# Performance work log

Measured on AMD Instinct MI355X. Metric: run time of the kernel, lower is better.

The kernel has to match this reference:

```python
import jax, jax.numpy as jnp
import numpy as np

N_NODES = 50000
N_EDGES = 300000
INPUT_DIM = 128
HIDDEN_DIM = 256
NUM_HEADS = 8
HEAD_DIM = HIDDEN_DIM // NUM_HEADS  # 32
NUM_EDGE_TYPES = 3


def setup_inputs() -> dict:
    key = jax.random.key(0)
    ks = jax.random.split(key, 12)
    s_in = 1.0 / np.sqrt(INPUT_DIM)
    s_hid = 1.0 / np.sqrt(HIDDEN_DIM)
    return {
        "node_features": jax.random.normal(ks[0], (N_NODES, INPUT_DIM), jnp.float32),
        "edges": jax.random.randint(ks[1], (N_EDGES, 2), 0, N_NODES),
        "edge_types": jax.random.randint(ks[2], (N_EDGES,), 0, NUM_EDGE_TYPES),
        # torch.nn.Linear convention: y = x @ W.T + b, W: [out, in]
        "Wq": jax.random.normal(ks[3], (HIDDEN_DIM, INPUT_DIM), jnp.float32) * s_in,
        "bq": jax.random.normal(ks[4], (HIDDEN_DIM,), jnp.float32) * s_in,
        "Wk": jax.random.normal(ks[5], (HIDDEN_DIM, INPUT_DIM), jnp.float32) * s_in,
        "bk": jax.random.normal(ks[6], (HIDDEN_DIM,), jnp.float32) * s_in,
        "Wv": jax.random.normal(ks[7], (HIDDEN_DIM, INPUT_DIM), jnp.float32) * s_in,
        "bv": jax.random.normal(ks[8], (HIDDEN_DIM,), jnp.float32) * s_in,
        "edge_emb": jax.random.normal(ks[9], (NUM_EDGE_TYPES, HIDDEN_DIM), jnp.float32),
        "Wo": jax.random.normal(ks[10], (INPUT_DIM, HIDDEN_DIM), jnp.float32) * s_hid,
        "bo": jax.random.normal(ks[11], (INPUT_DIM,), jnp.float32) * s_hid,
    }


def reference(node_features, edges, edge_types, Wq, bq, Wk, bk, Wv, bv, edge_emb, Wo, bo):
    # Project all nodes once, split heads: [N, H, D]
    Q = (node_features @ Wq.T + bq).reshape(-1, NUM_HEADS, HEAD_DIM)
    K = (node_features @ Wk.T + bk).reshape(-1, NUM_HEADS, HEAD_DIM)
    V = (node_features @ Wv.T + bv).reshape(-1, NUM_HEADS, HEAD_DIM)

    src = edges[:, 0]
    tgt = edges[:, 1]

    # Per-edge small attention: Q[src] [E,H,D] x K[tgt]^T -> [E,H,H]
    # (identical math to the original per-edge-type loop, since only the
    #  edge embedding depends on edge_type and it is gathered per edge)
    scale = 1.0 / jnp.sqrt(jnp.float32(HEAD_DIM))
    scores = jnp.einsum("ehd,egd->ehg", Q[src], K[tgt]) * scale
    attn = jax.nn.softmax(scores, axis=-1)
    msg = jnp.einsum("ehg,egd->ehd", attn, V[tgt]).reshape(-1, HIDDEN_DIM)  # [E, HID]

    msg = msg + edge_emb[edge_types]          # per-edge-type embedding add
    out_e = msg @ Wo.T + bo                   # output projection per edge [E, IN]

    # Scatter-add over source nodes (original Python loop over edges)
    messages = jax.ops.segment_sum(out_e, src, num_segments=N_NODES)
    return messages
```

## Files before the change

### kernel.cpp

```cpp
#include <hip/hip_runtime.h>
#include <hip/hip_bf16.h>

#define N_NODES 50000
#define N_EDGES 300000
#define M_PAD 50048
#define M_PAD2 50176
#define NBLK 196
#define SC 0.17677669529663687f

#define MB_CONV 6250
#define MB_HIST 1172
#define MB_PREP 513

#define QKV_BLOCKS 2346
#define SCAT_BLOCKS 586

typedef __attribute__((ext_vector_type(8))) short bf16x8;
typedef __attribute__((ext_vector_type(4))) short bf16x4;
typedef __attribute__((ext_vector_type(4))) float f32x4;

typedef __attribute__((address_space(3))) unsigned int lds_uint;
typedef const __attribute__((address_space(1))) unsigned int glb_uint;
__device__ __forceinline__ void gld16(const void* g, void* l) {
    __builtin_amdgcn_global_load_lds((glb_uint*)g, (lds_uint*)l, 16, 0, 0);
}

__device__ __forceinline__ unsigned short f2bf(float x) {
    unsigned int u = __float_as_uint(x);
    unsigned int r = (u + 0x7FFFu + ((u >> 16) & 1u)) >> 16;
    return (unsigned short)r;
}
__device__ __forceinline__ short bfs(float x) {
    __hip_bfloat16 h = __float2bfloat16(x);
    return *reinterpret_cast<short*>(&h);
}

__global__ __launch_bounds__(512)
void qkv_gemm(const unsigned short* __restrict__ A2, const unsigned short* __restrict__ B2,
              const float* __restrict__ biasCat,
              unsigned short* __restrict__ Qb, unsigned short* __restrict__ Kb,
              unsigned short* __restrict__ Vb,
              const int* __restrict__ edges, int* __restrict__ cursor,
              int* __restrict__ packed)
{
    __shared__ unsigned short SMEM[128 * 128];
    const int bid = blockIdx.x;
    const int t   = threadIdx.x;

    if (bid >= QKV_BLOCKS) {
        const int e = (bid - QKV_BLOCKS) * 512 + t;
        if (e < N_EDGES) {
            const int pos = atomicAdd(&cursor[edges[2 * e]], 1);
            packed[pos] = edges[2 * e + 1];
        }
        return;
    }

    const int w    = t >> 6;
    const int lane = t & 63;
    const int l15  = lane & 15;
    const int lg   = lane >> 4;
    const int mt   = bid % 6;
    const int mat  = mt % 3;
    const int nh   = mt / 3;
    const int m0   = (bid / 6) * 128;
    const int wm   = (w >> 2) * 64;
    const int wn   = (w & 3) * 32;
    const float mulc = (mat == 0) ? SC : 1.0f;

    {
        const char* srcbase = (const char*)A2 + (size_t)m0 * 256;
        #pragma unroll
        for (int i = 0; i < 4; ++i) {
            const int cb = (i * 8 + w) * 1024;
            gld16(srcbase + cb + lane * 16, (char*)SMEM + cb);
        }
    }

    f32x4 acc[4][2] = {};
    const unsigned short* Bbase =
        B2 + (size_t)(mat * 256 + nh * 128 + wn + l15) * 128 + lg * 8;

    __syncthreads();

    #pragma unroll
    for (int ks = 0; ks < 4; ++ks) {
        bf16x8 af[4], bfv[2];
        #pragma unroll
        for (int ni = 0; ni < 2; ++ni)
            bfv[ni] = *(const bf16x8*)(Bbase + (size_t)ni * 16 * 128 + ks * 32);
        #pragma unroll
        for (int mi = 0; mi < 4; ++mi) {
            const int r    = wm + mi * 16 + l15;
            const int slot = (ks * 4 + lg) ^ ((r & 7) << 1);
            af[mi] = *(const bf16x8*)((const char*)SMEM + r * 256 + slot * 16);
        }
        #pragma unroll
        for (int mi = 0; mi < 4; ++mi)
            #pragma unroll
            for (int ni = 0; ni < 2; ++ni)
                acc[mi][ni] = __builtin_amdgcn_mfma_f32_16x16x32_bf16(
                    af[mi], bfv[ni], acc[mi][ni], 0, 0, 0);
    }

    __syncthreads();

    unsigned short* Cs = SMEM;
    float bvn[2];
    #pragma unroll
    for (int ni = 0; ni < 2; ++ni)
        bvn[ni] = biasCat[mat * 256 + nh * 128 + wn + ni * 16 + l15];

    #pragma unroll
    for (int mi = 0; mi < 4; ++mi)
        #pragma unroll
        for (int j = 0; j < 4; ++j) {
            const int row = wm + mi * 16 + lg * 4 + j;
            const int xr  = (row & 7) << 3;
            #pragma unroll
            for (int ni = 0; ni < 2; ++ni) {
                const int col = wn + ni * 16 + l15;
                Cs[row * 128 + (col ^ xr)] = f2bf(fmaf(acc[mi][ni][j], mulc, bvn[ni]));
            }
        }
    __syncthreads();

    if (mat < 2) {
        unsigned short* dst = mat ? Kb : Qb;
        #pragma unroll
        for (int c8 = 0; c8 < 4; ++c8) {
            const int chunk = c8 * 512 + t;
            const int row = chunk >> 4;
            const int ec  = (chunk & 15) * 8;
            const bf16x8 v = *(const bf16x8*)&Cs[row * 128 + (ec ^ ((row & 7) << 3))];
            *(bf16x8*)&dst[(size_t)(m0 + row) * 256 + nh * 128 + ec] = v;
        }
    } else {
        #pragma unroll
        for (int i8 = 0; i8 < 8; ++i8) {
            const int item = i8 * 512 + t;
            const int row  = item >> 5;
            const int d    = item & 31;
            const int xr   = (row & 7) << 3;
            bf16x4 v;
            #pragma unroll
            for (int g = 0; g < 4; ++g)
                v[g] = (short)Cs[row * 128 + ((g * 32 + d) ^ xr)];
            *(bf16x4*)&Vb[(size_t)(m0 + row) * 256 + d * 8 + nh * 4] = v;
        }
    }
}

__global__ __launch_bounds__(128)
void out_gemm(const unsigned short* __restrict__ accQ, const unsigned short* __restrict__ B2o,
              const float* __restrict__ eew, const float* __restrict__ bo,
              const float4* __restrict__ cnt4, float* __restrict__ Cout)
{
    const int t    = threadIdx.x;
    const int w    = t >> 6;
    const int lane = t & 63;
    const int l15  = lane & 15;
    const int lg   = lane >> 4;
    const int m0   = blockIdx.y * 32;
    const int wn   = w * 64;

    f32x4 acc[2][4] = {};

    const unsigned short* Abase = accQ + (size_t)(m0 + l15) * 256 + lg * 8;
    const unsigned short* Bbase = B2o + (size_t)(wn + l15) * 256 + lg * 8;

    #pragma unroll 2
    for (int ks = 0; ks < 8; ++ks) {
        bf16x8 af[2], bfv[4];
        #pragma unroll
        for (int mi = 0; mi < 2; ++mi)
            af[mi] = *(const bf16x8*)(Abase + (size_t)mi * 16 * 256 + ks * 32);
        #pragma unroll
        for (int ni = 0; ni < 4; ++ni)
            bfv[ni] = *(const bf16x8*)(Bbase + (size_t)ni * 16 * 256 + ks * 32);
        #pragma unroll
        for (int mi = 0; mi < 2; ++mi)
            #pragma unroll
            for (int ni = 0; ni < 4; ++ni)
                acc[mi][ni] = __builtin_amdgcn_mfma_f32_16x16x32_bf16(
                    af[mi], bfv[ni], acc[mi][ni], 0, 0, 0);
    }

    #pragma unroll
    for (int mi = 0; mi < 2; ++mi)
        #pragma unroll
        for (int j = 0; j < 4; ++j) {
            const int row = m0 + mi * 16 + lg * 4 + j;
            if (row < N_NODES) {
                const float4 cv = cnt4[row];
                #pragma unroll
                for (int ni = 0; ni < 4; ++ni) {
                    const int col = wn + ni * 16 + l15;
                    Cout[(size_t)row * 128 + col] = acc[mi][ni][j]
                        + cv.x * eew[col] + cv.y * eew[128 + col]
                        + cv.z * eew[256 + col] + cv.w * bo[col];
                }
            }
        }
}

__global__ __launch_bounds__(256)
void mega_prep(const float4* __restrict__ nf4,
               const int* __restrict__ edges, const int* __restrict__ etypes,
               const float* __restrict__ Wq, const float* __restrict__ Wk,
               const float* __restrict__ Wv, const float* __restrict__ bq,
               const float* __restrict__ bk, const float* __restrict__ bv,
               const float* __restrict__ Wo, const float* __restrict__ ee,
               unsigned short* __restrict__ A2, unsigned short* __restrict__ B2qkv,
               unsigned short* __restrict__ B2o,
               float* __restrict__ biasCat, float* __restrict__ eew,
               int* __restrict__ degType)
{
    const int bid = blockIdx.x, t = threadIdx.x;
    if (bid < MB_CONV) {
        const int tid = bid * 256 + t;
        const int m = tid >> 5, k4 = (tid & 31) * 4;
        const float4 v = nf4[tid];
        ushort4 hi;
        hi.x = f2bf(v.x); hi.y = f2bf(v.y); hi.z = f2bf(v.z); hi.w = f2bf(v.w);
        const int chunk = k4 >> 3;
        const int sub   = k4 & 7;
        const int scol  = ((chunk ^ ((m & 7) << 1)) << 3) + sub;
        *reinterpret_cast<ushort4*>(&A2[(size_t)m * 128 + scol]) = hi;
    } else if (bid < MB_CONV + MB_HIST) {
        const int e = (bid - MB_CONV) * 256 + t;
        if (e < N_EDGES) atomicAdd(&degType[edges[2 * e] * 4 + etypes[e]], 1);
    } else {
        const int pbid = bid - MB_CONV - MB_HIST;
        if (pbid < 384) {
            const int tid = pbid * 256 + t;
            const int r = tid >> 7, k = tid & 127;
            const float* W = (r < 256) ? Wq : (r < 512) ? Wk : Wv;
            B2qkv[(size_t)r * 128 + k] = f2bf(W[(size_t)(r & 255) * 128 + k]);
            if (k == 0) {
                const float* b = (r < 256) ? bq : (r < 512) ? bk : bv;
                biasCat[r] = b[r & 255] * ((r < 256) ? SC : 1.0f);
            }
        } else if (pbid < 512) {
            const int tid = (pbid - 384) * 256 + t;
            const int r = tid >> 8, k = tid & 255;
            B2o[(size_t)r * 256 + k] = f2bf(Wo[(size_t)r * 256 + k]);
        } else if (t < 128) {
            float a0 = 0.f, a1 = 0.f, a2 = 0.f;
            for (int k = 0; k < 256; ++k) {
                const float w = Wo[(size_t)t * 256 + k];
                a0 += ee[k] * w; a1 += ee[256 + k] * w; a2 += ee[512 + k] * w;
            }
            eew[t] = a0; eew[128 + t] = a1; eew[256 + t] = a2;
        }
    }
}

__global__ __launch_bounds__(256)
void scan_part1(const int4* __restrict__ degType4, int* __restrict__ blockSum)
{
    const int t = threadIdx.x;
    const int i = blockIdx.x * 256 + t;
    int v = 0;
    if (i < N_NODES) {
        const int4 dt = degType4[i];
        v = dt.x + dt.y + dt.z;
    }
    #pragma unroll
    for (int o = 1; o < 64; o <<= 1) v += __shfl_xor(v, o);
    __shared__ int ws[4];
    if ((t & 63) == 0) ws[t >> 6] = v;
    __syncthreads();
    if (t == 0) blockSum[blockIdx.x] = ws[0] + ws[1] + ws[2] + ws[3];
}

__global__ __launch_bounds__(256)
void scan_part2(const int* __restrict__ blockSum, int* __restrict__ blockBase,
                int* __restrict__ rowStart)
{
    __shared__ int lds[256];
    const int t = threadIdx.x;
    lds[t] = (t < NBLK) ? blockSum[t] : 0;
    __syncthreads();
    #pragma unroll
    for (int o = 1; o < 256; o <<= 1) {
        const int u = (t >= o) ? lds[t - o] : 0;
        __syncthreads();
        lds[t] += u;
        __syncthreads();
    }
    if (t < NBLK) blockBase[t] = (t == 0) ? 0 : lds[t - 1];
    if (t == 0) rowStart[N_NODES] = N_EDGES;
}

__global__ __launch_bounds__(256)
void scan_part3(const int4* __restrict__ degType4, const int* __restrict__ blockBase,
                int* __restrict__ rowStart, int* __restrict__ cursor,
                float4* __restrict__ cnt4)
{
    const int t = threadIdx.x;
    const int lane = t & 63, wid = t >> 6;
    const int i = blockIdx.x * 256 + t;
    int4 dt = make_int4(0, 0, 0, 0);
    if (i < N_NODES) dt = degType4[i];
    const int d = dt.x + dt.y + dt.z;
    int x = d;
    #pragma unroll
    for (int o = 1; o < 64; o <<= 1) {
        const int u = __shfl_up(x, o);
        if (lane >= o) x += u;
    }
    __shared__ int wtot[4];
    if (lane == 63) wtot[wid] = x;
    __syncthreads();
    int wo = 0;
    #pragma unroll
    for (int wi = 0; wi < 3; ++wi) wo += (wi < wid) ? wtot[wi] : 0;
    const int excl = blockBase[blockIdx.x] + wo + x - d;
    if (i < N_NODES) {
        rowStart[i] = excl;
        cursor[i]   = excl;
        cnt4[i]     = make_float4((float)dt.x, (float)dt.y, (float)dt.z, (float)d);
    }
}

__device__ __forceinline__ bf16x4 softmax_pa(f32x4 s, bool valid)
{
    const float e0 = __expf(s[0]), e1 = __expf(s[1]);
    const float e2 = __expf(s[2]), e3 = __expf(s[3]);
    float sum = e0 + e1 + e2 + e3;
    sum += __shfl_xor(sum, 16);
    const float inv = valid ? __builtin_amdgcn_rcpf(sum) : 0.0f;
    bf16x4 pa;
    pa[0] = bfs(e0 * inv);
    pa[1] = bfs(e1 * inv);
    pa[2] = bfs(e2 * inv);
    pa[3] = bfs(e3 * inv);
    return pa;
}

__global__ __launch_bounds__(256)
void node_gather_kernel(const int* __restrict__ packed, const int* __restrict__ rowStart,
                        const unsigned short* __restrict__ Qb,
                        const unsigned short* __restrict__ Kb,
                        const unsigned short* __restrict__ Vb,
                        unsigned short* __restrict__ accQ)
{
    const int lane = threadIdx.x & 63;
    const int n = blockIdx.x * 4 + (threadIdx.x >> 6);
    if (n >= N_NODES) return;
    const int l15 = lane & 15;
    const int lg  = lane >> 4;

    const bf16x8 qf = *(const bf16x8*)&Qb[(size_t)n * 256 + (l15 & 7) * 32 + lg * 8];

    f32x4 cpvA0 = {0.f,0.f,0.f,0.f}, cpvA1 = {0.f,0.f,0.f,0.f};
    f32x4 cpvB0 = {0.f,0.f,0.f,0.f}, cpvB1 = {0.f,0.f,0.f,0.f};

    const int lo = rowStart[n], hi = rowStart[n + 1];
    const bool validBase = ((l15 < 8) == (lg < 2));
    const f32x4 z4 = {0.f, 0.f, 0.f, 0.f};
    int idx = lo;

    for (; idx + 4 <= hi; idx += 4) {
        const int t0 = packed[idx],     t1 = packed[idx + 1];
        const int t2 = packed[idx + 2], t3 = packed[idx + 3];

        const int tkA = (l15 < 8) ? t0 : t1;
        const int tkB = (l15 < 8) ? t2 : t3;
        const bf16x8 kfA = *(const bf16x8*)&Kb[(size_t)tkA * 256 + (l15 & 7) * 32 + lg * 8];
        const bf16x8 kfB = *(const bf16x8*)&Kb[(size_t)tkB * 256 + (l15 & 7) * 32 + lg * 8];

        const int tvA = (lg < 2) ? t0 : t1;
        const int tvB = (lg < 2) ? t2 : t3;
        const unsigned short* vrA = &Vb[(size_t)tvA * 256 + (lg & 1) * 4];
        const unsigned short* vrB = &Vb[(size_t)tvB * 256 + (lg & 1) * 4];
        const bf16x4 vfA0 = *(const bf16x4*)&vrA[l15 * 8];
        const bf16x4 vfA1 = *(const bf16x4*)&vrA[(l15 + 16) * 8];
        const bf16x4 vfB0 = *(const bf16x4*)&vrB[l15 * 8];
        const bf16x4 vfB1 = *(const bf16x4*)&vrB[(l15 + 16) * 8];

        const f32x4 sA = __builtin_amdgcn_mfma_f32_16x16x32_bf16(kfA, qf, z4, 0, 0, 0);
        const f32x4 sB = __builtin_amdgcn_mfma_f32_16x16x32_bf16(kfB, qf, z4, 0, 0, 0);

        const bf16x4 paA = softmax_pa(sA, validBase);
        const bf16x4 paB = softmax_pa(sB, validBase);

        cpvA0 = __builtin_amdgcn_mfma_f32_16x16x16bf16_1k(paA, vfA0, cpvA0, 0, 0, 0);
        cpvA1 = __builtin_amdgcn_mfma_f32_16x16x16bf16_1k(paA, vfA1, cpvA1, 0, 0, 0);
        cpvB0 = __builtin_amdgcn_mfma_f32_16x16x16bf16_1k(paB, vfB0, cpvB0, 0, 0, 0);
        cpvB1 = __builtin_amdgcn_mfma_f32_16x16x16bf16_1k(paB, vfB1, cpvB1, 0, 0, 0);
    }

    for (; idx < hi; idx += 2) {
        const int  t0  = packed[idx];
        const bool dup = (idx + 1 >= hi);
        const int  t1  = dup ? t0 : packed[idx + 1];

        const int tk = (l15 < 8) ? t0 : t1;
        const bf16x8 kf = *(const bf16x8*)&Kb[(size_t)tk * 256 + (l15 & 7) * 32 + lg * 8];

        const int tv = (lg < 2) ? t0 : t1;
        const unsigned short* vrow = &Vb[(size_t)tv * 256 + (lg & 1) * 4];
        const bf16x4 vf0 = *(const bf16x4*)&vrow[l15 * 8];
        const bf16x4 vf1 = *(const bf16x4*)&vrow[(l15 + 16) * 8];

        const f32x4 s = __builtin_amdgcn_mfma_f32_16x16x32_bf16(kf, qf, z4, 0, 0, 0);
        const bool valid = validBase && !(dup && (l15 >= 8));
        const bf16x4 pa = softmax_pa(s, valid);

        cpvA0 = __builtin_amdgcn_mfma_f32_16x16x16bf16_1k(pa, vf0, cpvA0, 0, 0, 0);
        cpvA1 = __builtin_amdgcn_mfma_f32_16x16x16bf16_1k(pa, vf1, cpvA1, 0, 0, 0);
    }

    f32x4 cpv0 = cpvA0 + cpvB0;
    f32x4 cpv1 = cpvA1 + cpvB1;

    #pragma unroll
    for (int j = 0; j < 4; ++j) {
        cpv0[j] += __shfl_xor(cpv0[j], 32);
        cpv1[j] += __shfl_xor(cpv1[j], 32);
    }

    if (lane < 32) {
        unsigned short* row = &accQ[(size_t)n * 256];
        #pragma unroll
        for (int j = 0; j < 4; ++j) {
            const int h = lg * 4 + j;
            row[h * 32 + l15]      = (unsigned short)bfs(cpv0[j]);
            row[h * 32 + 16 + l15] = (unsigned short)bfs(cpv1[j]);
        }
    }
}

extern "C" void kernel_launch(void* const* d_in, const int* in_sizes, int n_in,
                              void* d_out, int out_size, void* d_ws, size_t ws_size,
                              hipStream_t stream)
{
    const float* nf      = (const float*)d_in[0];
    const int*   edges   = (const int*)d_in[1];
    const int*   etypes  = (const int*)d_in[2];
    const float* Wq      = (const float*)d_in[3];
    const float* bq      = (const float*)d_in[4];
    const float* Wk      = (const float*)d_in[5];
    const float* bk      = (const float*)d_in[6];
    const float* Wv      = (const float*)d_in[7];
    const float* bv      = (const float*)d_in[8];
    const float* ee      = (const float*)d_in[9];
    const float* Wo      = (const float*)d_in[10];
    const float* bo      = (const float*)d_in[11];
    float* out = (float*)d_out;

    char* ws = (char*)d_ws;
    size_t off = 0;
    auto alloc = [&](size_t bytes) -> void* {
        void* p = ws + off;
        off = (off + bytes + 255) & ~(size_t)255;
        return p;
    };
    unsigned short* A2     = (unsigned short*)alloc((size_t)M_PAD * 128 * 2);
    unsigned short* B2qkv  = (unsigned short*)alloc((size_t)768 * 128 * 2);
    unsigned short* B2o    = (unsigned short*)alloc((size_t)128 * 256 * 2);
    float*          biasC  = (float*)alloc(768 * sizeof(float));
    float*          eew    = (float*)alloc(384 * sizeof(float));
    unsigned short* Qb     = (unsigned short*)alloc((size_t)M_PAD * 256 * 2);
    unsigned short* Kb     = (unsigned short*)alloc((size_t)M_PAD * 256 * 2);
    unsigned short* Vb     = (unsigned short*)alloc((size_t)M_PAD * 256 * 2);
    unsigned short* accQ   = (unsigned short*)alloc((size_t)M_PAD2 * 256 * 2);
    float4* cnt4    = (float4*)alloc((size_t)N_NODES * sizeof(float4));
    int*    degType = (int*)alloc((size_t)N_NODES * 4 * sizeof(int));
    int*    rowS    = (int*)alloc((size_t)(N_NODES + 1) * sizeof(int));
    int*    curs    = (int*)alloc((size_t)N_NODES * sizeof(int));
    int*    pck     = (int*)alloc((size_t)N_EDGES * sizeof(int));
    int*    bSum    = (int*)alloc((size_t)NBLK * sizeof(int));
    int*    bBase   = (int*)alloc((size_t)NBLK * sizeof(int));

    const dim3 blk(256);

    hipMemsetAsync(degType, 0, (size_t)N_NODES * 4 * sizeof(int), stream);
    mega_prep<<<dim3(MB_CONV + MB_HIST + MB_PREP), blk, 0, stream>>>(
        (const float4*)nf, edges, etypes, Wq, Wk, Wv, bq, bk, bv, Wo, ee,
        A2, B2qkv, B2o, biasC, eew, degType);

    scan_part1<<<dim3(NBLK), blk, 0, stream>>>((const int4*)degType, bSum);
    scan_part2<<<dim3(1), blk, 0, stream>>>(bSum, bBase, rowS);
    scan_part3<<<dim3(NBLK), blk, 0, stream>>>((const int4*)degType, bBase, rowS, curs, cnt4);

    qkv_gemm<<<dim3(QKV_BLOCKS + SCAT_BLOCKS), dim3(512), 0, stream>>>(
        A2, B2qkv, biasC, Qb, Kb, Vb, edges, curs, pck);

    node_gather_kernel<<<dim3((N_NODES + 3) / 4), blk, 0, stream>>>(
        pck, rowS, Qb, Kb, Vb, accQ);

    out_gemm<<<dim3(1, M_PAD2 / 32), dim3(128), 0, stream>>>(
        accQ, B2o, eew, bo, cnt4, out);
}
```

Measured before the change: 161.5 us.

## Loop all six QKV tiles per 64-row block and repack V for 16-byte gathers

New measurement: 162.7 us. Within noise of the previous version (+0.7%).

```diff
diff --git a/kernel.cpp b/kernel.cpp
--- a/kernel.cpp
+++ b/kernel.cpp
@@ -12,7 +12,7 @@
 #define MB_HIST 1172
 #define MB_PREP 513
 
-#define QKV_BLOCKS 2346
+#define QKV_BLOCKS 782
 #define SCAT_BLOCKS 586
 
 typedef __attribute__((ext_vector_type(8))) short bf16x8;
@@ -43,7 +43,8 @@
               const int* __restrict__ edges, int* __restrict__ cursor,
               int* __restrict__ packed)
 {
-    __shared__ unsigned short SMEM[128 * 128];
+    __shared__ unsigned short A_s[64 * 128];
+    __shared__ unsigned short C_s[64 * 128];
     const int bid = blockIdx.x;
     const int t   = threadIdx.x;
 
@@ -60,93 +61,77 @@
     const int lane = t & 63;
     const int l15  = lane & 15;
     const int lg   = lane >> 4;
-    const int mt   = bid % 6;
-    const int mat  = mt % 3;
-    const int nh   = mt / 3;
-    const int m0   = (bid / 6) * 128;
-    const int wm   = (w >> 2) * 64;
-    const int wn   = (w & 3) * 32;
-    const float mulc = (mat == 0) ? SC : 1.0f;
+    const int m0   = bid * 64;
+    const int wn   = w * 16;
 
     {
         const char* srcbase = (const char*)A2 + (size_t)m0 * 256;
-        #pragma unroll
-        for (int i = 0; i < 4; ++i) {
-            const int cb = (i * 8 + w) * 1024;
-            gld16(srcbase + cb + lane * 16, (char*)SMEM + cb);
-        }
-    }
-
-    f32x4 acc[4][2] = {};
-    const unsigned short* Bbase =
-        B2 + (size_t)(mat * 256 + nh * 128 + wn + l15) * 128 + lg * 8;
-
+        gld16(srcbase + t * 16,              (char*)A_s + t * 16);
+        gld16(srcbase + (512 + t) * 16,      (char*)A_s + (512 + t) * 16);
+    }
     __syncthreads();
 
     #pragma unroll
-    for (int ks = 0; ks < 4; ++ks) {
-        bf16x8 af[4], bfv[2];
-        #pragma unroll
-        for (int ni = 0; ni < 2; ++ni)
-            bfv[ni] = *(const bf16x8*)(Bbase + (size_t)ni * 16 * 128 + ks * 32);
-        #pragma unroll
-        for (int mi = 0; mi < 4; ++mi) {
-            const int r    = wm + mi * 16 + l15;
-            const int slot = (ks * 4 + lg) ^ ((r & 7) << 1);
-            af[mi] = *(const bf16x8*)((const char*)SMEM + r * 256 + slot * 16);
-        }
+    for (int mt = 0; mt < 6; ++mt) {
+        const int mat = mt >> 1;
+        const int nh  = mt & 1;
+        const float mulc = (mat == 0) ? SC : 1.0f;
+        const float bvn  = biasCat[mat * 256 + nh * 128 + wn + l15];
+        const unsigned short* Bbase =
+            B2 + (size_t)(mat * 256 + nh * 128 + wn + l15) * 128 + lg * 8;
+
+        f32x4 acc[4] = {};
+        #pragma unroll
+        for (int ks = 0; ks < 4; ++ks) {
+            const bf16x8 bfv = *(const bf16x8*)(Bbase + ks * 32);
+            #pragma unroll
+            for (int mi = 0; mi < 4; ++mi) {
+                const int r    = mi * 16 + l15;
+                const int slot = (ks * 4 + lg) ^ ((r & 7) << 1);
+                const bf16x8 af = *(const bf16x8*)((const char*)A_s + r * 256 + slot * 16);
+                acc[mi] = __builtin_amdgcn_mfma_f32_16x16x32_bf16(af, bfv, acc[mi], 0, 0, 0);
+            }
+        }
+
+        __syncthreads();
+
         #pragma unroll
         for (int mi = 0; mi < 4; ++mi)
             #pragma unroll
-            for (int ni = 0; ni < 2; ++ni)
-                acc[mi][ni] = __builtin_amdgcn_mfma_f32_16x16x32_bf16(
-                    af[mi], bfv[ni], acc[mi][ni], 0, 0, 0);
-    }
-
-    __syncthreads();
-
-    unsigned short* Cs = SMEM;
-    float bvn[2];
-    #pragma unroll
-    for (int ni = 0; ni < 2; ++ni)
-        bvn[ni] = biasCat[mat * 256 + nh * 128 + wn + ni * 16 + l15];
-
-    #pragma unroll
-    for (int mi = 0; mi < 4; ++mi)
-        #pragma unroll
-        for (int j = 0; j < 4; ++j) {
-            const int row = wm + mi * 16 + lg * 4 + j;
-            const int xr  = (row & 7) << 3;
+            for (int j = 0; j < 4; ++j) {
+                const int row = mi * 16 + lg * 4 + j;
+                const int xr  = (row & 7) << 3;
+                const int col = wn + l15;
+                C_s[row * 128 + (col ^ xr)] = f2bf(fmaf(acc[mi][j], mulc, bvn));
+            }
+        __syncthreads();
+
+        if (mat < 2) {
+            unsigned short* dst = mat ? Kb : Qb;
             #pragma unroll
-            for (int ni = 0; ni < 2; ++ni) {
-                const int col = wn + ni * 16 + l15;
-                Cs[row * 128 + (col ^ xr)] = f2bf(fmaf(acc[mi][ni][j], mulc, bvn[ni]));
-            }
-        }
-    __syncthreads();
-
-    if (mat < 2) {
-        unsigned short* dst = mat ? Kb : Qb;
-        #pragma unroll
-        for (int c8 = 0; c8 < 4; ++c8) {
-            const int chunk = c8 * 512 + t;
-            const int row = chunk >> 4;
-            const int ec  = (chunk & 15) * 8;
-            const bf16x8 v = *(const bf16x8*)&Cs[row * 128 + (ec ^ ((row & 7) << 3))];
-            *(bf16x8*)&dst[(size_t)(m0 + row) * 256 + nh * 128 + ec] = v;
-        }
-    } else {
-        #pragma unroll
-        for (int i8 = 0; i8 < 8; ++i8) {
-            const int item = i8 * 512 + t;
-            const int row  = item >> 5;
-            const int d    = item & 31;
-            const int xr   = (row & 7) << 3;
-            bf16x4 v;
+            for (int c8 = 0; c8 < 2; ++c8) {
+                const int chunk = c8 * 512 + t;
+                const int row = chunk >> 4;
+                const int ec  = (chunk & 15) * 8;
+                const bf16x8 v = *(const bf16x8*)&C_s[row * 128 + (ec ^ ((row & 7) << 3))];
+                *(bf16x8*)&dst[(size_t)(m0 + row) * 256 + nh * 128 + ec] = v;
+            }
+        } else {
             #pragma unroll
-            for (int g = 0; g < 4; ++g)
-                v[g] = (short)Cs[row * 128 + ((g * 32 + d) ^ xr)];
-            *(bf16x4*)&Vb[(size_t)(m0 + row) * 256 + d * 8 + nh * 4] = v;
+            for (int c8 = 0; c8 < 2; ++c8) {
+                const int item = c8 * 512 + t;
+                const int row  = item >> 4;
+                const int dlow = item & 15;
+                const int xr   = (row & 7) << 3;
+                bf16x8 v;
+                #pragma unroll
+                for (int jp = 0; jp < 8; ++jp) {
+                    const int dhi = jp >> 2, gp = jp & 3;
+                    const int cp  = gp * 32 + dlow + 16 * dhi;
+                    v[jp] = (short)C_s[row * 128 + (cp ^ xr)];
+                }
+                *(bf16x8*)&Vb[(size_t)(m0 + row) * 256 + nh * 128 + dlow * 8] = v;
+            }
         }
     }
 }
@@ -339,6 +324,8 @@
     return pa;
 }
 
+union v8split { bf16x8 v8; bf16x4 h[2]; };
+
 __global__ __launch_bounds__(256)
 void node_gather_kernel(const int* __restrict__ packed, const int* __restrict__ rowStart,
                         const unsigned short* __restrict__ Qb,
@@ -360,6 +347,7 @@
     const int lo = rowStart[n], hi = rowStart[n + 1];
     const bool validBase = ((l15 < 8) == (lg < 2));
     const f32x4 z4 = {0.f, 0.f, 0.f, 0.f};
+    const int voff = (lg & 1) * 128 + l15 * 8;
     int idx = lo;
 
     for (; idx + 4 <= hi; idx += 4) {
@@ -373,12 +361,9 @@
 
         const int tvA = (lg < 2) ? t0 : t1;
         const int tvB = (lg < 2) ? t2 : t3;
-        const unsigned short* vrA = &Vb[(size_t)tvA * 256 + (lg & 1) * 4];
-        const unsigned short* vrB = &Vb[(size_t)tvB * 256 + (lg & 1) * 4];
-        const bf16x4 vfA0 = *(const bf16x4*)&vrA[l15 * 8];
-        const bf16x4 vfA1 = *(const bf16x4*)&vrA[(l15 + 16) * 8];
-        const bf16x4 vfB0 = *(const bf16x4*)&vrB[l15 * 8];
-        const bf16x4 vfB1 = *(const bf16x4*)&vrB[(l15 + 16) * 8];
+        v8split vA, vB;
+        vA.v8 = *(const bf16x8*)&Vb[(size_t)tvA * 256 + voff];
+        vB.v8 = *(const bf16x8*)&Vb[(size_t)tvB * 256 + voff];
 
         const f32x4 sA = __builtin_amdgcn_mfma_f32_16x16x32_bf16(kfA, qf, z4, 0, 0, 0);
         const f32x4 sB = __builtin_amdgcn_mfma_f32_16x16x32_bf16(kfB, qf, z4, 0, 0, 0);
@@ -386,10 +371,10 @@
         const bf16x4 paA = softmax_pa(sA, validBase);
         const bf16x4 paB = softmax_pa(sB, validBase);
 
-        cpvA0 = __builtin_amdgcn_mfma_f32_16x16x16bf16_1k(paA, vfA0, cpvA0, 0, 0, 0);
-        cpvA1 = __builtin_amdgcn_mfma_f32_16x16x16bf16_1k(paA, vfA1, cpvA1, 0, 0, 0);
-        cpvB0 = __builtin_amdgcn_mfma_f32_16x16x16bf16_1k(paB, vfB0, cpvB0, 0, 0, 0);
-        cpvB1 = __builtin_amdgcn_mfma_f32_16x16x16bf16_1k(paB, vfB1, cpvB1, 0, 0, 0);
+        cpvA0 = __builtin_amdgcn_mfma_f32_16x16x16bf16_1k(paA, vA.h[0], cpvA0, 0, 0, 0);
+        cpvA1 = __builtin_amdgcn_mfma_f32_16x16x16bf16_1k(paA, vA.h[1], cpvA1, 0, 0, 0);
+        cpvB0 = __builtin_amdgcn_mfma_f32_16x16x16bf16_1k(paB, vB.h[0], cpvB0, 0, 0, 0);
+        cpvB1 = __builtin_amdgcn_mfma_f32_16x16x16bf16_1k(paB, vB.h[1], cpvB1, 0, 0, 0);
     }
 
     for (; idx < hi; idx += 2) {
@@ -401,16 +386,15 @@
         const bf16x8 kf = *(const bf16x8*)&Kb[(size_t)tk * 256 + (l15 & 7) * 32 + lg * 8];
 
         const int tv = (lg < 2) ? t0 : t1;
-        const unsigned short* vrow = &Vb[(size_t)tv * 256 + (lg & 1) * 4];
-        const bf16x4 vf0 = *(const bf16x4*)&vrow[l15 * 8];
-        const bf16x4 vf1 = *(const bf16x4*)&vrow[(l15 + 16) * 8];
+        v8split vA;
+        vA.v8 = *(const bf16x8*)&Vb[(size_t)tv * 256 + voff];
 
         const f32x4 s = __builtin_amdgcn_mfma_f32_16x16x32_bf16(kf, qf, z4, 0, 0, 0);
         const bool valid = validBase && !(dup && (l15 >= 8));
         const bf16x4 pa = softmax_pa(s, valid);
 
-        cpvA0 = __builtin_amdgcn_mfma_f32_16x16x16bf16_1k(pa, vf0, cpvA0, 0, 0, 0);
-        cpvA1 = __builtin_amdgcn_mfma_f32_16x16x16bf16_1k(pa, vf1, cpvA1, 0, 0, 0);
+        cpvA0 = __builtin_amdgcn_mfma_f32_16x16x16bf16_1k(pa, vA.h[0], cpvA0, 0, 0, 0);
+        cpvA1 = __builtin_amdgcn_mfma_f32_16x16x16bf16_1k(pa, vA.h[1], cpvA1, 0, 0, 0);
     }
 
     f32x4 cpv0 = cpvA0 + cpvB0;
```
